# Optimization experiments

Hardware: AMD Instinct MI355X
Metric: run time of the kernel (lower is better)

The kernel has to match this reference:

```python
import jax, jax.numpy as jnp
import numpy as np
import math

L, B, T, D, H, F = 4, 4, 2048, 1024, 1024, 256
R_MIN, R_MAX = 0.9, 0.99
MAX_PHASE = math.pi / 50  # hardcoded in LRU.__init__


def setup_inputs() -> dict:
    key = jax.random.key(0)
    ks = iter(jax.random.split(key, 32))
    inputs = jax.random.normal(next(ks), (B, T, F), dtype=jnp.float32)
    # input projection (torch Linear layout: W [out,in])
    lim = 1.0 / math.sqrt(F)
    W_in = jax.random.uniform(next(ks), (D, F), minval=-lim, maxval=lim, dtype=jnp.float32)
    b_in = jax.random.uniform(next(ks), (D,), minval=-lim, maxval=lim, dtype=jnp.float32)
    # per-layer LRU params (stacked over layer dim)
    u1 = jax.random.uniform(next(ks), (L, H), dtype=jnp.float32) * (1 - 1e-5) + 1e-5
    mag_sq = u1 * (R_MAX ** 2 - R_MIN ** 2) + R_MIN ** 2
    nu_log = jnp.log(-0.5 * jnp.log(mag_sq + 1e-5))
    u2 = jax.random.uniform(next(ks), (L, H), dtype=jnp.float32) * (1 - 1e-5) + 1e-5
    theta_log = jnp.log(MAX_PHASE * u2)
    B_re = jax.random.normal(next(ks), (L, H, D), dtype=jnp.float32) / math.sqrt(2 * D)
    B_im = jax.random.normal(next(ks), (L, H, D), dtype=jnp.float32) / math.sqrt(2 * D)
    C_re = jax.random.normal(next(ks), (L, D, H), dtype=jnp.float32) / math.sqrt(H)
    C_im = jax.random.normal(next(ks), (L, D, H), dtype=jnp.float32) / math.sqrt(H)
    D_diag = jax.random.normal(next(ks), (L, D), dtype=jnp.float32)
    # LayerNorm affine
    ln_scale = jnp.ones((L, D), dtype=jnp.float32)
    ln_bias = jnp.zeros((L, D), dtype=jnp.float32)
    # GLU output linears (torch layout [out,in])
    limd = 1.0 / math.sqrt(D)
    w1 = jax.random.uniform(next(ks), (L, D, D), minval=-limd, maxval=limd, dtype=jnp.float32)
    b1 = jax.random.uniform(next(ks), (L, D), minval=-limd, maxval=limd, dtype=jnp.float32)
    w2 = jax.random.uniform(next(ks), (L, D, D), minval=-limd, maxval=limd, dtype=jnp.float32)
    b2 = jax.random.uniform(next(ks), (L, D), minval=-limd, maxval=limd, dtype=jnp.float32)
    return {"inputs": inputs, "W_in": W_in, "b_in": b_in, "nu_log": nu_log,
            "theta_log": theta_log, "B_re": B_re, "B_im": B_im, "C_re": C_re,
            "C_im": C_im, "D_diag": D_diag, "ln_scale": ln_scale, "ln_bias": ln_bias,
            "w1": w1, "b1": b1, "w2": w2, "b2": b2}


def _layernorm(x, scale, bias, eps=1e-5):
    mu = jnp.mean(x, axis=-1, keepdims=True)
    var = jnp.mean((x - mu) ** 2, axis=-1, keepdims=True)
    return (x - mu) * jax.lax.rsqrt(var + eps) * scale + bias


def _lru(x, nu_log, theta_log, B_re, B_im, C_re, C_im, D_diag):
    # x: [B,T,D] real -> [B,T,D] real
    nu = jnp.exp(nu_log)
    theta = jnp.exp(theta_log)
    lam = jnp.exp(-nu + 1j * theta)                        # [H] complex
    # gamma recomputed from nu_log each forward (matches torch code)
    gamma = jnp.exp(0.5 * jnp.log(1 - jnp.exp(-2 * nu) + 1e-5))
    B_norm = (B_re + 1j * B_im) * gamma[:, None]           # [H,D]
    Bu = jnp.einsum('hd,btd->bth', B_norm, x.astype(jnp.complex64))  # [B,T,H]

    def step(h, bu):
        h = lam * h + bu
        return h, h

    h0 = jnp.zeros((x.shape[0], lam.shape[0]), dtype=jnp.complex64)
    _, hs = jax.lax.scan(step, h0, jnp.swapaxes(Bu, 0, 1))  # [T,B,H]
    hs = jnp.swapaxes(hs, 0, 1)                             # [B,T,H]
    C = C_re + 1j * C_im                                    # [D,H]
    y = jnp.einsum('bth,dh->btd', hs, C).real + x * D_diag
    return y.astype(jnp.float32)


def reference(inputs, W_in, b_in, nu_log, theta_log, B_re, B_im, C_re, C_im,
              D_diag, ln_scale, ln_bias, w1, b1, w2, b2):
    x = inputs @ W_in.T + b_in                              # [B,T,D]
    n_layers = nu_log.shape[0]
    for l in range(n_layers):
        xn = _layernorm(x, ln_scale[l], ln_bias[l])
        y = _lru(xn, nu_log[l], theta_log[l], B_re[l], B_im[l],
                 C_re[l], C_im[l], D_diag[l])
        y = jax.nn.gelu(y, approximate=False)
        y = (y @ w1[l].T + b1[l]) * jax.nn.sigmoid(y @ w2[l].T + b2[l])
        x = x + y
    return x
```

## Files before the change

kernel.cpp:

```cpp
#include <hip/hip_runtime.h>
#include <hip/hip_bf16.h>
#include <math.h>

typedef unsigned short u16;
typedef short s16x8 __attribute__((ext_vector_type(8)));
typedef float f32x4 __attribute__((ext_vector_type(4)));
typedef unsigned short u16x4 __attribute__((ext_vector_type(4)));

#define NLAYER 4
#define BB 4
#define TT 2048
#define DD 1024
#define HH 1024
#define FF 256
#define MM 8192
#define CL 64
#define NC 32
#define PLANE 4096
#define STPLANE 131072

__device__ __forceinline__ u16 f2bf(float f) {
  __hip_bfloat16 h = __float2bfloat16(f);
  return __builtin_bit_cast(u16, h);
}
__device__ __forceinline__ float bf2f(u16 u) {
  __hip_bfloat16 h = __builtin_bit_cast(__hip_bfloat16, u);
  return __bfloat162float(h);
}

__global__ __launch_bounds__(256) void params_kernel(
    const float* __restrict__ nu_log, const float* __restrict__ theta_log,
    float* __restrict__ P) {
  int i = blockIdx.x * 256 + threadIdx.x;
  if (i >= PLANE) return;
  float nu = expf(nu_log[i]);
  float th = expf(theta_log[i]);
  float r = expf(-nu);
  P[i]           = r * cosf(th);
  P[PLANE + i]   = r * sinf(th);
  P[2*PLANE + i] = sqrtf(1.f - expf(-2.f * nu) + 1e-5f);
  float rC = expf(-(float)CL * nu);
  float thC = (float)CL * th;
  P[3*PLANE + i] = rC * cosf(thC);
  P[4*PLANE + i] = rC * sinf(thC);
}

__global__ __launch_bounds__(256) void f2bf_kernel(
    const float* __restrict__ src, u16* __restrict__ dst, int n) {
  int i = blockIdx.x * 256 + threadIdx.x;
  if (i < n) dst[i] = f2bf(src[i]);
}

__global__ __launch_bounds__(256) void conv_layer_kernel(
    const float* __restrict__ Bre, const float* __restrict__ Bim,
    const float* __restrict__ Cre, const float* __restrict__ Cim,
    const float* __restrict__ w1, const float* __restrict__ w2,
    const float* __restrict__ gamma,
    u16* __restrict__ wBn, u16* __restrict__ wC,
    u16* __restrict__ w1b, u16* __restrict__ w2b) {
  int idx = blockIdx.x * 256 + threadIdx.x;
  if (idx < 2097152) {
    int n = idx >> 10, d = idx & 1023;
    float v = (n < 1024) ? Bre[n * 1024 + d] * gamma[n]
                         : Bim[(n - 1024) * 1024 + d] * gamma[n - 1024];
    wBn[idx] = f2bf(v);
  } else if (idx < 4194304) {
    int i = idx - 2097152;
    int d = i >> 11, k = i & 2047;
    float v = (k < 1024) ? Cre[d * 1024 + k] : -Cim[d * 1024 + (k - 1024)];
    wC[i] = f2bf(v);
  } else if (idx < 5242880) {
    int i = idx - 4194304;
    w1b[i] = f2bf(w1[i]);
  } else if (idx < 6291456) {
    int i = idx - 5242880;
    w2b[i] = f2bf(w2[i]);
  }
}

__global__ __launch_bounds__(256) void ln_kernel(
    const float* __restrict__ x, const float* __restrict__ sc,
    const float* __restrict__ bi, u16* __restrict__ xn) {
  const int row = blockIdx.x;
  const int tid = threadIdx.x;
  const float4 v = ((const float4*)(x + (size_t)row * 1024))[tid];
  float s = v.x + v.y + v.z + v.w;
  float ss = v.x * v.x + v.y * v.y + v.z * v.z + v.w * v.w;
  __shared__ float r1[256], r2[256];
  r1[tid] = s; r2[tid] = ss;
  __syncthreads();
  for (int stp = 128; stp > 0; stp >>= 1) {
    if (tid < stp) { r1[tid] += r1[tid + stp]; r2[tid] += r2[tid + stp]; }
    __syncthreads();
  }
  const float mu = r1[0] * 0.0009765625f;
  const float var = r2[0] * 0.0009765625f - mu * mu;
  const float inv = rsqrtf(var + 1e-5f);
  const int c = tid * 4;
  u16x4 o;
  o.x = f2bf((v.x - mu) * inv * sc[c]     + bi[c]);
  o.y = f2bf((v.y - mu) * inv * sc[c + 1] + bi[c + 1]);
  o.z = f2bf((v.z - mu) * inv * sc[c + 2] + bi[c + 2]);
  o.w = f2bf((v.w - mu) * inv * sc[c + 3] + bi[c + 3]);
  *(u16x4*)&xn[(size_t)row * 1024 + c] = o;
}

__global__ __launch_bounds__(256) void scanA_kernel(
    u16* __restrict__ Bu, const float* __restrict__ P, float* __restrict__ st,
    int l) {
  const int tid = blockIdx.x * 256 + threadIdx.x;
  const int h2 = tid & 511;
  const int c = (tid >> 9) & 31;
  const int b = tid >> 14;
  const int h = h2 * 2;
  const float lr0 = P[l * 1024 + h],     li0 = P[PLANE + l * 1024 + h];
  const float lr1 = P[l * 1024 + h + 1], li1 = P[PLANE + l * 1024 + h + 1];
  const size_t base = ((size_t)(b * TT + c * CL)) * 2048 + h;
  float h0r = 0.f, h0i = 0.f, h1r = 0.f, h1i = 0.f;
  for (int j = 0; j < CL; j++) {
    size_t o = base + (size_t)j * 2048;
    uint re2 = *(const uint*)(Bu + o);
    uint im2 = *(const uint*)(Bu + o + 1024);
    float b0r = bf2f((u16)(re2 & 0xffffu)), b1r = bf2f((u16)(re2 >> 16));
    float b0i = bf2f((u16)(im2 & 0xffffu)), b1i = bf2f((u16)(im2 >> 16));
    float t0r = lr0 * h0r - li0 * h0i + b0r;
    float t0i = lr0 * h0i + li0 * h0r + b0i;
    float t1r = lr1 * h1r - li1 * h1i + b1r;
    float t1i = lr1 * h1i + li1 * h1r + b1i;
    h0r = t0r; h0i = t0i; h1r = t1r; h1i = t1i;
    *(uint*)(Bu + o)        = (uint)f2bf(h0r) | ((uint)f2bf(h1r) << 16);
    *(uint*)(Bu + o + 1024) = (uint)f2bf(h0i) | ((uint)f2bf(h1i) << 16);
  }
  size_t si = ((size_t)(b * NC + c)) * 1024 + h;
  st[si] = h0r; st[si + 1] = h1r;
  st[STPLANE + si] = h0i; st[STPLANE + si + 1] = h1i;
}

__global__ __launch_bounds__(256) void scanB_kernel(
    float* __restrict__ st, const float* __restrict__ P, int l) {
  const int tid = blockIdx.x * 256 + threadIdx.x;
  const int h = tid & 1023;
  const int b = tid >> 10;
  const float cr = P[3*PLANE + l * 1024 + h], ci = P[4*PLANE + l * 1024 + h];
  float pr = 0.f, pi = 0.f;
  for (int c = 0; c < NC; c++) {
    size_t i = ((size_t)(b * NC + c)) * 1024 + h;
    float sr = st[i], sim = st[STPLANE + i];
    st[i] = pr; st[STPLANE + i] = pi;
    float nr = cr * pr - ci * pi + sr;
    float ni = cr * pi + ci * pr + sim;
    pr = nr; pi = ni;
  }
}

__global__ __launch_bounds__(256) void scanC_kernel(
    u16* __restrict__ Bu, const float* __restrict__ P,
    const float* __restrict__ st, int l) {
  const int tid = blockIdx.x * 256 + threadIdx.x;
  const int h2 = tid & 511;
  const int c = (tid >> 9) & 31;
  const int b = tid >> 14;
  if (c == 0) return;
  const int h = h2 * 2;
  const float lr0 = P[l * 1024 + h],     li0 = P[PLANE + l * 1024 + h];
  const float lr1 = P[l * 1024 + h + 1], li1 = P[PLANE + l * 1024 + h + 1];
  size_t si = ((size_t)(b * NC + c)) * 1024 + h;
  float q0r = st[si], q1r = st[si + 1];
  float q0i = st[STPLANE + si], q1i = st[STPLANE + si + 1];
  const size_t base = ((size_t)(b * TT + c * CL)) * 2048 + h;
  for (int j = 0; j < CL; j++) {
    float t0r = lr0 * q0r - li0 * q0i;
    float t0i = lr0 * q0i + li0 * q0r;
    float t1r = lr1 * q1r - li1 * q1i;
    float t1i = lr1 * q1i + li1 * q1r;
    q0r = t0r; q0i = t0i; q1r = t1r; q1i = t1i;
    size_t o = base + (size_t)j * 2048;
    uint re2 = *(const uint*)(Bu + o);
    uint im2 = *(const uint*)(Bu + o + 1024);
    float v0r = bf2f((u16)(re2 & 0xffffu)) + q0r;
    float v1r = bf2f((u16)(re2 >> 16))     + q1r;
    float v0i = bf2f((u16)(im2 & 0xffffu)) + q0i;
    float v1i = bf2f((u16)(im2 >> 16))     + q1i;
    *(uint*)(Bu + o)        = (uint)f2bf(v0r) | ((uint)f2bf(v1r) << 16);
    *(uint*)(Bu + o + 1024) = (uint)f2bf(v0i) | ((uint)f2bf(v1i) << 16);
  }
}

__device__ __forceinline__ void stage32(const u16* __restrict__ gbase,
                                        int row_stride, u16* lds_base,
                                        int wave, int lane) {
  const int r8 = lane >> 3;
  const int c8 = (lane & 7) * 8;
  #pragma unroll
  for (int i = 0; i < 4; i++) {
    const int rbase = wave * 32 + i * 8;
    const u16* g = gbase + (size_t)(rbase + r8) * row_stride + c8;
    u16* l = lds_base + rbase * 64;
    __builtin_amdgcn_global_load_lds(
        (const __attribute__((address_space(1))) void*)g,
        (__attribute__((address_space(3))) void*)l, 16, 0, 0);
  }
}

template <int MODE>
__global__ __launch_bounds__(256, 2) void gemm_kernel(
    const u16* __restrict__ A, const u16* __restrict__ W,
    const u16* __restrict__ W2, int K, int N, void* __restrict__ outp,
    const float* __restrict__ bias, const float* __restrict__ bias2,
    const float* __restrict__ ddiag, const u16* __restrict__ xnp) {
  __shared__ u16 As[128 * 64];
  __shared__ u16 Bs[128 * 64];
  __shared__ u16 Bs2[(MODE == 3) ? 128 * 64 : 64];

  const int tid = threadIdx.x;
  const int m0 = blockIdx.x * 128;
  const int n0 = blockIdx.y * 128;
  const int wave = tid >> 6;
  const int lane = tid & 63;
  const int wm = wave & 1;
  const int wn = wave >> 1;
  const int lr = lane & 15;
  const int quad = lane >> 4;

  f32x4 acc[4][4];
  f32x4 acc2[4][4];
  #pragma unroll
  for (int i = 0; i < 4; i++)
    #pragma unroll
    for (int j = 0; j < 4; j++)
      #pragma unroll
      for (int r = 0; r < 4; r++) {
        acc[i][j][r] = 0.f;
        if constexpr (MODE == 3) acc2[i][j][r] = 0.f;
      }

  for (int kb = 0; kb < K; kb += 64) {
    stage32(A + (size_t)m0 * K + kb, K, As, wave, lane);
    stage32(W + (size_t)n0 * K + kb, K, Bs, wave, lane);
    if constexpr (MODE == 3)
      stage32(W2 + (size_t)n0 * K + kb, K, Bs2, wave, lane);
    __syncthreads();
    #pragma unroll
    for (int ks = 0; ks < 2; ks++) {
      s16x8 af[4], bfr[4], bfr2[4];
      #pragma unroll
      for (int t = 0; t < 4; t++) {
        af[t]  = *(const s16x8*)&As[(wm * 64 + t * 16 + lr) * 64 + ks * 32 + quad * 8];
        bfr[t] = *(const s16x8*)&Bs[(wn * 64 + t * 16 + lr) * 64 + ks * 32 + quad * 8];
        if constexpr (MODE == 3)
          bfr2[t] = *(const s16x8*)&Bs2[(wn * 64 + t * 16 + lr) * 64 + ks * 32 + quad * 8];
      }
      #pragma unroll
      for (int mt = 0; mt < 4; mt++)
        #pragma unroll
        for (int nt = 0; nt < 4; nt++) {
          acc[mt][nt] = __builtin_amdgcn_mfma_f32_16x16x32_bf16(
              af[mt], bfr[nt], acc[mt][nt], 0, 0, 0);
          if constexpr (MODE == 3)
            acc2[mt][nt] = __builtin_amdgcn_mfma_f32_16x16x32_bf16(
                af[mt], bfr2[nt], acc2[mt][nt], 0, 0, 0);
        }
    }
    __syncthreads();
  }

  const int mbase = m0 + wm * 64 + quad * 4;
  const int nbase = n0 + wn * 64 + lr;
  #pragma unroll
  for (int mt = 0; mt < 4; mt++)
    #pragma unroll
    for (int nt = 0; nt < 4; nt++) {
      const int n = nbase + nt * 16;
      #pragma unroll
      for (int r = 0; r < 4; r++) {
        const int m = mbase + mt * 16 + r;
        const float v = acc[mt][nt][r];
        if constexpr (MODE == 0) {
          ((u16*)outp)[(size_t)m * N + n] = f2bf(v);
        } else if constexpr (MODE == 1) {
          ((float*)outp)[(size_t)m * N + n] = v + bias[n];
        } else if constexpr (MODE == 2) {
          float t = v + bf2f(xnp[(size_t)m * 1024 + n]) * ddiag[n];
          float g = t * 0.5f * (1.f + erff(t * 0.70710678118f));
          ((u16*)outp)[(size_t)m * N + n] = f2bf(g);
        } else {
          float a = v + bias[n];
          float g2 = acc2[mt][nt][r] + bias2[n];
          float sig = 1.f / (1.f + expf(-g2));
          float* xp = (float*)outp;
          xp[(size_t)m * N + n] += a * sig;
        }
      }
    }
}

extern "C" void kernel_launch(void* const* d_in, const int* in_sizes, int n_in,
                              void* d_out, int out_size, void* d_ws,
                              size_t ws_size, hipStream_t stream) {
  const float* inputs    = (const float*)d_in[0];
  const float* W_in      = (const float*)d_in[1];
  const float* b_in      = (const float*)d_in[2];
  const float* nu_log    = (const float*)d_in[3];
  const float* theta_log = (const float*)d_in[4];
  const float* B_re      = (const float*)d_in[5];
  const float* B_im      = (const float*)d_in[6];
  const float* C_re      = (const float*)d_in[7];
  const float* C_im      = (const float*)d_in[8];
  const float* D_diag    = (const float*)d_in[9];
  const float* ln_s      = (const float*)d_in[10];
  const float* ln_b      = (const float*)d_in[11];
  const float* w1        = (const float*)d_in[12];
  const float* b1        = (const float*)d_in[13];
  const float* w2        = (const float*)d_in[14];
  const float* b2        = (const float*)d_in[15];
  float* x = (float*)d_out;

  char* p = (char*)d_ws;
  auto alloc = [&](size_t bytes) -> char* {
    char* r = p;
    p += (bytes + 255) & ~(size_t)255;
    return r;
  };
  float* P       = (float*)alloc(5 * PLANE * 4);
  u16* inputs_bf = (u16*)alloc((size_t)MM * FF * 2);
  u16* Win_bf    = (u16*)alloc((size_t)DD * FF * 2);
  u16* xn        = (u16*)alloc((size_t)MM * DD * 2);
  u16* Bu        = (u16*)alloc((size_t)MM * 2048 * 2);
  u16* yg        = (u16*)alloc((size_t)MM * DD * 2);
  float* st      = (float*)alloc(2 * (size_t)STPLANE * 4);
  u16* wBn       = (u16*)alloc((size_t)2048 * 1024 * 2);
  u16* wC        = (u16*)alloc((size_t)1024 * 2048 * 2);
  u16* w1b       = (u16*)alloc((size_t)1024 * 1024 * 2);
  u16* w2b       = (u16*)alloc((size_t)1024 * 1024 * 2);

  params_kernel<<<16, 256, 0, stream>>>(nu_log, theta_log, P);
  f2bf_kernel<<<(MM * FF + 255) / 256, 256, 0, stream>>>(inputs, inputs_bf, MM * FF);
  f2bf_kernel<<<(DD * FF + 255) / 256, 256, 0, stream>>>(W_in, Win_bf, DD * FF);

  gemm_kernel<1><<<dim3(64, 8), 256, 0, stream>>>(
      inputs_bf, Win_bf, nullptr, FF, DD, x, b_in, nullptr, nullptr, nullptr);

  for (int l = 0; l < NLAYER; l++) {
    ln_kernel<<<MM, 256, 0, stream>>>(x, ln_s + l * 1024, ln_b + l * 1024, xn);
    conv_layer_kernel<<<24576, 256, 0, stream>>>(
        B_re + (size_t)l * 1048576, B_im + (size_t)l * 1048576,
        C_re + (size_t)l * 1048576, C_im + (size_t)l * 1048576,
        w1 + (size_t)l * 1048576, w2 + (size_t)l * 1048576,
        P + 2 * PLANE + l * 1024, wBn, wC, w1b, w2b);
    gemm_kernel<0><<<dim3(64, 16), 256, 0, stream>>>(
        xn, wBn, nullptr, DD, 2048, Bu, nullptr, nullptr, nullptr, nullptr);
    scanA_kernel<<<256, 256, 0, stream>>>(Bu, P, st, l);
    scanB_kernel<<<16, 256, 0, stream>>>(st, P, l);
    scanC_kernel<<<256, 256, 0, stream>>>(Bu, P, st, l);
    gemm_kernel<2><<<dim3(64, 8), 256, 0, stream>>>(
        Bu, wC, nullptr, 2048, DD, yg, nullptr, nullptr, D_diag + l * 1024, xn);
    gemm_kernel<3><<<dim3(64, 8), 256, 0, stream>>>(
        yg, w1b, w2b, DD, DD, x, b1 + l * 1024, b2 + l * 1024, nullptr, nullptr);
  }
}
```

Measured before the change: 1.088 ms.

## Halve GEMM N-tile to 64 and XOR-swizzle LDS staging to avoid bank conflicts

Shrinks the GEMM block tile from 128x128 to 128x64 and doubles the grid in N, so more blocks fill the GPU and fewer accumulator registers are needed; launch bounds rise to 4 blocks per CU. Global-to-LDS staging now permutes 16-byte column chunks by an XOR with the row index, and fragment reads apply the same swizzle to cut LDS bank conflicts. The cost is less reuse of each A tile per block, so A traffic from global memory and L2 roughly doubles.

```diff
diff --git a/kernel.cpp b/kernel.cpp
--- a/kernel.cpp
+++ b/kernel.cpp
@@ -186,15 +186,17 @@
   }
 }
 
-__device__ __forceinline__ void stage32(const u16* __restrict__ gbase,
-                                        int row_stride, u16* lds_base,
-                                        int wave, int lane) {
+__device__ __forceinline__ void stage_rows(const u16* __restrict__ gbase,
+                                           int row_stride, u16* lds_base,
+                                           int rows_per_wave, int wave,
+                                           int lane) {
   const int r8 = lane >> 3;
-  const int c8 = (lane & 7) * 8;
+  const int slot = lane & 7;
+  const int gc = (slot ^ r8) * 8;
   #pragma unroll
-  for (int i = 0; i < 4; i++) {
-    const int rbase = wave * 32 + i * 8;
-    const u16* g = gbase + (size_t)(rbase + r8) * row_stride + c8;
+  for (int i = 0; i < rows_per_wave / 8; i++) {
+    const int rbase = wave * rows_per_wave + i * 8;
+    const u16* g = gbase + (size_t)(rbase + r8) * row_stride + gc;
     u16* l = lds_base + rbase * 64;
     __builtin_amdgcn_global_load_lds(
         (const __attribute__((address_space(1))) void*)g,
@@ -203,31 +205,32 @@
 }
 
 template <int MODE>
-__global__ __launch_bounds__(256, 2) void gemm_kernel(
+__global__ __launch_bounds__(256, 4) void gemm_kernel(
     const u16* __restrict__ A, const u16* __restrict__ W,
     const u16* __restrict__ W2, int K, int N, void* __restrict__ outp,
     const float* __restrict__ bias, const float* __restrict__ bias2,
     const float* __restrict__ ddiag, const u16* __restrict__ xnp) {
   __shared__ u16 As[128 * 64];
-  __shared__ u16 Bs[128 * 64];
-  __shared__ u16 Bs2[(MODE == 3) ? 128 * 64 : 64];
+  __shared__ u16 Bs[64 * 64];
+  __shared__ u16 Bs2[(MODE == 3) ? 64 * 64 : 64];
 
   const int tid = threadIdx.x;
   const int m0 = blockIdx.x * 128;
-  const int n0 = blockIdx.y * 128;
+  const int n0 = blockIdx.y * 64;
   const int wave = tid >> 6;
   const int lane = tid & 63;
   const int wm = wave & 1;
   const int wn = wave >> 1;
   const int lr = lane & 15;
   const int quad = lane >> 4;
-
-  f32x4 acc[4][4];
-  f32x4 acc2[4][4];
+  const int sw = lr & 7;
+
+  f32x4 acc[4][2];
+  f32x4 acc2[4][2];
   #pragma unroll
   for (int i = 0; i < 4; i++)
     #pragma unroll
-    for (int j = 0; j < 4; j++)
+    for (int j = 0; j < 2; j++)
       #pragma unroll
       for (int r = 0; r < 4; r++) {
         acc[i][j][r] = 0.f;
@@ -235,25 +238,28 @@
       }
 
   for (int kb = 0; kb < K; kb += 64) {
-    stage32(A + (size_t)m0 * K + kb, K, As, wave, lane);
-    stage32(W + (size_t)n0 * K + kb, K, Bs, wave, lane);
+    stage_rows(A + (size_t)m0 * K + kb, K, As, 32, wave, lane);
+    stage_rows(W + (size_t)n0 * K + kb, K, Bs, 16, wave, lane);
     if constexpr (MODE == 3)
-      stage32(W2 + (size_t)n0 * K + kb, K, Bs2, wave, lane);
+      stage_rows(W2 + (size_t)n0 * K + kb, K, Bs2, 16, wave, lane);
     __syncthreads();
     #pragma unroll
     for (int ks = 0; ks < 2; ks++) {
-      s16x8 af[4], bfr[4], bfr2[4];
-      #pragma unroll
-      for (int t = 0; t < 4; t++) {
-        af[t]  = *(const s16x8*)&As[(wm * 64 + t * 16 + lr) * 64 + ks * 32 + quad * 8];
-        bfr[t] = *(const s16x8*)&Bs[(wn * 64 + t * 16 + lr) * 64 + ks * 32 + quad * 8];
+      const int cslot = ((ks * 4 + quad) ^ sw) * 8;
+      s16x8 af[4], bfr[2], bfr2[2];
+      #pragma unroll
+      for (int t = 0; t < 4; t++)
+        af[t] = *(const s16x8*)&As[(wm * 64 + t * 16 + lr) * 64 + cslot];
+      #pragma unroll
+      for (int t = 0; t < 2; t++) {
+        bfr[t] = *(const s16x8*)&Bs[(wn * 32 + t * 16 + lr) * 64 + cslot];
         if constexpr (MODE == 3)
-          bfr2[t] = *(const s16x8*)&Bs2[(wn * 64 + t * 16 + lr) * 64 + ks * 32 + quad * 8];
+          bfr2[t] = *(const s16x8*)&Bs2[(wn * 32 + t * 16 + lr) * 64 + cslot];
       }
       #pragma unroll
       for (int mt = 0; mt < 4; mt++)
         #pragma unroll
-        for (int nt = 0; nt < 4; nt++) {
+        for (int nt = 0; nt < 2; nt++) {
           acc[mt][nt] = __builtin_amdgcn_mfma_f32_16x16x32_bf16(
               af[mt], bfr[nt], acc[mt][nt], 0, 0, 0);
           if constexpr (MODE == 3)
@@ -265,11 +271,11 @@
   }
 
   const int mbase = m0 + wm * 64 + quad * 4;
-  const int nbase = n0 + wn * 64 + lr;
+  const int nbase = n0 + wn * 32 + lr;
   #pragma unroll
   for (int mt = 0; mt < 4; mt++)
     #pragma unroll
-    for (int nt = 0; nt < 4; nt++) {
+    for (int nt = 0; nt < 2; nt++) {
       const int n = nbase + nt * 16;
       #pragma unroll
       for (int r = 0; r < 4; r++) {
@@ -337,7 +343,7 @@
   f2bf_kernel<<<(MM * FF + 255) / 256, 256, 0, stream>>>(inputs, inputs_bf, MM * FF);
   f2bf_kernel<<<(DD * FF + 255) / 256, 256, 0, stream>>>(W_in, Win_bf, DD * FF);
 
-  gemm_kernel<1><<<dim3(64, 8), 256, 0, stream>>>(
+  gemm_kernel<1><<<dim3(64, 16), 256, 0, stream>>>(
       inputs_bf, Win_bf, nullptr, FF, DD, x, b_in, nullptr, nullptr, nullptr);
 
   for (int l = 0; l < NLAYER; l++) {
@@ -347,14 +353,14 @@
         C_re + (size_t)l * 1048576, C_im + (size_t)l * 1048576,
         w1 + (size_t)l * 1048576, w2 + (size_t)l * 1048576,
         P + 2 * PLANE + l * 1024, wBn, wC, w1b, w2b);
-    gemm_kernel<0><<<dim3(64, 16), 256, 0, stream>>>(
+    gemm_kernel<0><<<dim3(64, 32), 256, 0, stream>>>(
         xn, wBn, nullptr, DD, 2048, Bu, nullptr, nullptr, nullptr, nullptr);
     scanA_kernel<<<256, 256, 0, stream>>>(Bu, P, st, l);
     scanB_kernel<<<16, 256, 0, stream>>>(st, P, l);
     scanC_kernel<<<256, 256, 0, stream>>>(Bu, P, st, l);
-    gemm_kernel<2><<<dim3(64, 8), 256, 0, stream>>>(
+    gemm_kernel<2><<<dim3(64, 16), 256, 0, stream>>>(
         Bu, wC, nullptr, 2048, DD, yg, nullptr, nullptr, D_diag + l * 1024, xn);
-    gemm_kernel<3><<<dim3(64, 8), 256, 0, stream>>>(
+    gemm_kernel<3><<<dim3(64, 16), 256, 0, stream>>>(
         yg, w1b, w2b, DD, DD, x, b1 + l * 1024, b2 + l * 1024, nullptr, nullptr);
   }
 }
```

Result: faster. 954.5 us (-12.2%).
